# Optimization experiments

Measured on AMD Instinct MI355X. Metric: run time of the kernel, lower is better.

## Reference

```python
import jax, jax.numpy as jnp
import numpy as np

D, H, W = 256, 256, 256
R = 6                      # max_radius: per-Gaussian half-window in voxels


def setup_inputs() -> dict:
    key = jax.random.key(0)
    k1, k2, k3, k4, k5 = jax.random.split(key, 5)
    N = 20000
    center_vox = jax.random.uniform(k1, (N, 3), minval=float(R), maxval=float(D - R), dtype=jnp.float32)
    A = jax.random.normal(k2, (N, 3, 3), dtype=jnp.float32) * 0.5
    # SPD inverse covariance in normalized coords (diffs divided by half_shape ~128)
    cov_inv = (jnp.einsum('nij,nkj->nik', A, A) + jnp.eye(3, dtype=jnp.float32)) * 2000.0
    density_r = jax.random.normal(k3, (N,), dtype=jnp.float32)
    density_i = jax.random.normal(k4, (N,), dtype=jnp.float32)
    radius_vox = jax.random.uniform(k5, (N,), minval=3.0, maxval=float(R), dtype=jnp.float32)
    half_shape = jnp.array([D / 2.0, H / 2.0, W / 2.0], dtype=jnp.float32)
    return {
        'center_vox': center_vox,
        'cov_inv': cov_inv,
        'density_r': density_r,
        'density_i': density_i,
        'radius_vox': radius_vox,
        'half_shape': half_shape,
    }


def reference(center_vox, cov_inv, density_r, density_i, radius_vox, half_shape):
    # Per-Gaussian fixed window of side (2R+1); gather -> Mahalanobis weight -> scatter-add.
    offs = jnp.arange(-R, R + 1, dtype=jnp.int32)
    od, oh, ow = jnp.meshgrid(offs, offs, offs, indexing='ij')
    off = jnp.stack([od, oh, ow], axis=-1).reshape(-1, 3)          # [K3,3]
    base = jnp.floor(center_vox).astype(jnp.int32)                  # [N,3]
    vox = base[:, None, :] + off[None, :, :]                        # [N,K3,3] int
    voxf = vox.astype(center_vox.dtype)
    diff = (voxf - center_vox[:, None, :]) / half_shape             # normalized diff [N,K3,3]
    Md = jnp.einsum('nkd,nde,nke->nk', diff, cov_inv, diff)         # Mahalanobis [N,K3]
    # bbox mask (floor(c-r) .. ceil(c+r)) as in build_tile_pairs / CUDA kernel
    bmin = jnp.floor(center_vox - radius_vox[:, None])
    bmax = jnp.ceil(center_vox + radius_vox[:, None])
    in_bbox = jnp.all((voxf >= bmin[:, None, :]) & (voxf <= bmax[:, None, :]), axis=-1)
    dims = jnp.array([D, H, W], dtype=jnp.int32)
    in_grid = jnp.all((vox >= 0) & (vox < dims), axis=-1)
    mask = (Md <= 9.0) & in_bbox & in_grid
    w = jnp.exp(-0.5 * Md) * mask.astype(Md.dtype)                  # [N,K3]
    flat = jnp.where(in_grid, vox[..., 0] * (H * W) + vox[..., 1] * W + vox[..., 2], 0).reshape(-1)
    vol_r = jnp.zeros(D * H * W, dtype=w.dtype).at[flat].add((w * density_r[:, None]).reshape(-1))
    vol_i = jnp.zeros(D * H * W, dtype=w.dtype).at[flat].add((w * density_i[:, None]).reshape(-1))
    return vol_r.reshape(D, H, W), vol_i.reshape(D, H, W)
```

## Files before the change

kernel.cpp:

```cpp
#include <hip/hip_runtime.h>

#define DD 256
#define HH 256
#define WW 256
#define RMAX 6

#define NTILES 65536
#define CAP 24
#define RECSZ 16
#define OVF_CAP 8192

__global__ __launch_bounds__(256) void fill_kernel(
    const float* __restrict__ center, const float* __restrict__ cov_inv,
    const float* __restrict__ dens_r, const float* __restrict__ dens_i,
    const float* __restrict__ radius, const float* __restrict__ half_shape,
    int* __restrict__ tile_cnt, float* __restrict__ tile_recs,
    int* __restrict__ ovf_cnt, int* __restrict__ ovf_list, int N)
{
    int lane = threadIdx.x & 63;
    int i = __builtin_amdgcn_readfirstlane(blockIdx.x * 4 + (threadIdx.x >> 6));
    if (i >= N) return;

    float cx = center[3*i+0], cy = center[3*i+1], cz = center[3*i+2];
    float r  = radius[i];
    float c00=cov_inv[9*i+0], c01=cov_inv[9*i+1], c02=cov_inv[9*i+2];
    float c11=cov_inv[9*i+4], c12=cov_inv[9*i+5], c22=cov_inv[9*i+8];

    float d00 = c11*c22 - c12*c12;
    float d11 = c00*c22 - c02*c02;
    float d22 = c00*c11 - c01*c01;
    float det = c00*d00 - c01*(c01*c22 - c02*c12) + c02*(c01*c12 - c02*c11);
    float k9  = 9.0f / det;
    float hx = half_shape[0], hy = half_shape[1], hz = half_shape[2];
    float ex = hx * sqrtf(d00 * k9) * 1.0001f + 0.01f;
    float ey = hy * sqrtf(d11 * k9) * 1.0001f + 0.01f;
    float ez = hz * sqrtf(d22 * k9) * 1.0001f + 0.01f;
    float rx = fminf(r, ex), ry = fminf(r, ey), rz = fminf(r, ez);

    int bx=(int)floorf(cx), by=(int)floorf(cy), bz=(int)floorf(cz);
    int xlo = max(max((int)floorf(cx - rx), bx - RMAX), 0);
    int xhi = min(min((int)ceilf (cx + rx), bx + RMAX), DD - 1);
    int ylo = max(max((int)floorf(cy - ry), by - RMAX), 0);
    int yhi = min(min((int)ceilf (cy + ry), by + RMAX), HH - 1);
    int zlo = max(max((int)floorf(cz - rz), bz - RMAX), 0);
    int zhi = min(min((int)ceilf (cz + rz), bz + RMAX), WW - 1);
    if (xlo > xhi || ylo > yhi || zlo > zhi) return;

    int tx0 = xlo >> 2, ntx = (xhi >> 2) - tx0 + 1;
    int ty0 = ylo >> 2, nty = (yhi >> 2) - ty0 + 1;
    int tz0 = zlo >> 4, ntz = (zhi >> 4) - tz0 + 1;
    int ntiles = ntx * nty * ntz;

    if (lane >= ntiles) return;

    unsigned lo = (unsigned)xlo | ((unsigned)ylo << 8) | ((unsigned)zlo << 16);
    unsigned hi = (unsigned)xhi | ((unsigned)yhi << 8) | ((unsigned)zhi << 16);
    float4 r0 = make_float4(cx, cy, cz, c00);
    float4 r1 = make_float4(c11, c22, c01 + c01, c02 + c02);
    float4 r2 = make_float4(c12 + c12, dens_r[i], dens_i[i], __uint_as_float(lo));
    float4 r3 = make_float4(__uint_as_float(hi), 0.f, 0.f, 0.f);

    int t = lane;
    int tzz = tz0 + (t % ntz); t /= ntz;
    int tyy = ty0 + (t % nty); t /= nty;
    int txx = tx0 + t;
    int tile = (txx << 10) | (tyy << 4) | tzz;

    int pos = atomicAdd(&tile_cnt[tile], 1);
    if (pos < CAP) {
        float4* R = (float4*)(tile_recs + ((size_t)tile * CAP + pos) * RECSZ);
        R[0] = r0; R[1] = r1; R[2] = r2; R[3] = r3;
    } else {
        int o = atomicAdd(ovf_cnt, 1);
        if (o < OVF_CAP) { ovf_list[2*o] = tile; ovf_list[2*o+1] = i; }
    }
}

__global__ __launch_bounds__(256) void gather_kernel(
    const int* __restrict__ tile_cnt, const float* __restrict__ tile_recs,
    const float* __restrict__ half_shape,
    float* __restrict__ vol_r, float* __restrict__ vol_i)
{
    __shared__ float4 lds[4 * CAP * 4];
    int w = threadIdx.x >> 6, lane = threadIdx.x & 63;
    int tile = (blockIdx.x << 2) | w;
    int tz = tile & 15, ty = (tile >> 4) & 63, tx = tile >> 10;
    int dxl = lane >> 4, dyl = (lane >> 2) & 3, dzq = lane & 3;
    int vx = tx*4 + dxl, vy = ty*4 + dyl, vz0 = tz*16 + dzq*4;
    float vxf = (float)vx, vyf = (float)vy, vz0f = (float)vz0;
    float ihx = 1.0f/half_shape[0], ihy = 1.0f/half_shape[1], ihz = 1.0f/half_shape[2];

    int n = min(tile_cnt[tile], CAP);
    float4* wl = lds + w * (CAP * 4);
    const float4* src = (const float4*)(tile_recs + (size_t)tile * CAP * RECSZ);
    for (int idx = lane; idx < n * 4; idx += 64) wl[idx] = src[idx];

    float ar0=0.f, ar1=0.f, ar2=0.f, ar3=0.f;
    float ai0=0.f, ai1=0.f, ai2=0.f, ai3=0.f;

    for (int j = 0; j < n; ++j) {
        float4 r0 = wl[j*4+0];
        float4 r1 = wl[j*4+1];
        float4 r2 = wl[j*4+2];
        float4 r3 = wl[j*4+3];
        float cx=r0.x, cy=r0.y, cz=r0.z, s00=r0.w;
        float s11=r1.x, s22=r1.y, s01=r1.z, s02=r1.w;
        float s12=r2.x, dr=r2.y, di=r2.z;
        unsigned lo = __float_as_uint(r2.w), hi = __float_as_uint(r3.x);
        int xlo = lo & 255, ylo = (lo >> 8) & 255, zlo = (lo >> 16) & 255;
        int xhi = hi & 255, yhi = (hi >> 8) & 255, zhi = (hi >> 16) & 255;

        bool okxy = ((unsigned)(vx - xlo) <= (unsigned)(xhi - xlo)) &
                    ((unsigned)(vy - ylo) <= (unsigned)(yhi - ylo));
        int iz0 = vz0 - zlo;
        unsigned zspan = (unsigned)(zhi - zlo);

        float fx = (vxf - cx) * ihx;
        float fy = (vyf - cy) * ihy;
        float axy = fx*fx*s00 + fx*fy*s01 + fy*fy*s11;
        float bxy = fx*s02 + fy*s12;
        float nczihz = -cz * ihz;

        float fz0 = fmaf(vz0f, ihz, nczihz);
        float fz1 = fz0 + ihz;
        float fz2 = fz1 + ihz;
        float fz3 = fz2 + ihz;
        float md0 = fmaf(fz0, fmaf(s22, fz0, bxy), axy);
        float md1 = fmaf(fz1, fmaf(s22, fz1, bxy), axy);
        float md2 = fmaf(fz2, fmaf(s22, fz2, bxy), axy);
        float md3 = fmaf(fz3, fmaf(s22, fz3, bxy), axy);

        bool ok0 = okxy & ((unsigned)(iz0    ) <= zspan) & (md0 <= 9.0f);
        bool ok1 = okxy & ((unsigned)(iz0 + 1) <= zspan) & (md1 <= 9.0f);
        bool ok2 = okxy & ((unsigned)(iz0 + 2) <= zspan) & (md2 <= 9.0f);
        bool ok3 = okxy & ((unsigned)(iz0 + 3) <= zspan) & (md3 <= 9.0f);

        if (__any(ok0 | ok1 | ok2 | ok3)) {
            const float kexp = -0.72134752044448169f;
            float w0 = ok0 ? exp2f(md0 * kexp) : 0.0f;
            float w1 = ok1 ? exp2f(md1 * kexp) : 0.0f;
            float w2 = ok2 ? exp2f(md2 * kexp) : 0.0f;
            float w3 = ok3 ? exp2f(md3 * kexp) : 0.0f;
            ar0 = fmaf(w0, dr, ar0); ai0 = fmaf(w0, di, ai0);
            ar1 = fmaf(w1, dr, ar1); ai1 = fmaf(w1, di, ai1);
            ar2 = fmaf(w2, dr, ar2); ai2 = fmaf(w2, di, ai2);
            ar3 = fmaf(w3, dr, ar3); ai3 = fmaf(w3, di, ai3);
        }
    }

    size_t flat = ((size_t)vx * HH + vy) * WW + vz0;
    *(float4*)(vol_r + flat) = make_float4(ar0, ar1, ar2, ar3);
    *(float4*)(vol_i + flat) = make_float4(ai0, ai1, ai2, ai3);
}

__global__ __launch_bounds__(64) void ovf_kernel(
    const int* __restrict__ ovf_cnt, const int* __restrict__ ovf_list,
    const float* __restrict__ center, const float* __restrict__ cov_inv,
    const float* __restrict__ dens_r, const float* __restrict__ dens_i,
    const float* __restrict__ radius, const float* __restrict__ half_shape,
    float* __restrict__ vol_r, float* __restrict__ vol_i)
{
    int total = min(ovf_cnt[0], OVF_CAP);
    float ihx = 1.0f/half_shape[0], ihy = 1.0f/half_shape[1], ihz = 1.0f/half_shape[2];
    int lane = threadIdx.x;
    for (int p = blockIdx.x; p < total; p += gridDim.x) {
        int tile = ovf_list[2*p], g = ovf_list[2*p+1];
        int tz = tile & 15, ty = (tile >> 4) & 63, tx = tile >> 10;
        int dxl = lane >> 4, dyl = (lane >> 2) & 3, dzq = lane & 3;
        int vx = tx*4 + dxl, vy = ty*4 + dyl, vz0 = tz*16 + dzq*4;

        float cx = center[3*g+0], cy = center[3*g+1], cz = center[3*g+2];
        float r  = radius[g];
        float c00=cov_inv[9*g+0], c01=cov_inv[9*g+1], c02=cov_inv[9*g+2];
        float c10=cov_inv[9*g+3], c11=cov_inv[9*g+4], c12=cov_inv[9*g+5];
        float c20=cov_inv[9*g+6], c21=cov_inv[9*g+7], c22=cov_inv[9*g+8];
        float dr = dens_r[g], di = dens_i[g];

        int bx=(int)floorf(cx), by=(int)floorf(cy), bz=(int)floorf(cz);
        int xlo = max(max((int)floorf(cx - r), bx - RMAX), 0);
        int xhi = min(min((int)ceilf (cx + r), bx + RMAX), DD - 1);
        int ylo = max(max((int)floorf(cy - r), by - RMAX), 0);
        int yhi = min(min((int)ceilf (cy + r), by + RMAX), HH - 1);
        int zlo = max(max((int)floorf(cz - r), bz - RMAX), 0);
        int zhi = min(min((int)ceilf (cz + r), bz + RMAX), WW - 1);

        if (vx < xlo || vx > xhi || vy < ylo || vy > yhi) continue;
        float fx = ((float)vx - cx) * ihx;
        float fy = ((float)vy - cy) * ihy;
        for (int k = 0; k < 4; ++k) {
            int vz = vz0 + k;
            float fz = ((float)vz - cz) * ihz;
            float md = fx*(c00*fx + c01*fy + c02*fz)
                     + fy*(c10*fx + c11*fy + c12*fz)
                     + fz*(c20*fx + c21*fy + c22*fz);
            if (vz >= zlo && vz <= zhi && md <= 9.0f) {
                float wgt = __expf(-0.5f * md);
                size_t flat = ((size_t)vx * HH + vy) * WW + vz;
                atomicAdd(&vol_r[flat], wgt * dr);
                atomicAdd(&vol_i[flat], wgt * di);
            }
        }
    }
}

__global__ __launch_bounds__(256) void splat_kernel(
    const float* __restrict__ center, const float* __restrict__ cov_inv,
    const float* __restrict__ dens_r, const float* __restrict__ dens_i,
    const float* __restrict__ radius, const float* __restrict__ half_shape,
    float* __restrict__ vol_r, float* __restrict__ vol_i, int N)
{
    int g = blockIdx.x;
    if (g >= N) return;
    float cx = center[3*g+0], cy = center[3*g+1], cz = center[3*g+2];
    float r  = radius[g];
    float c00 = cov_inv[9*g+0], c01 = cov_inv[9*g+1], c02 = cov_inv[9*g+2];
    float c10 = cov_inv[9*g+3], c11 = cov_inv[9*g+4], c12 = cov_inv[9*g+5];
    float c20 = cov_inv[9*g+6], c21 = cov_inv[9*g+7], c22 = cov_inv[9*g+8];
    float dr = dens_r[g], di = dens_i[g];
    float ihx = 1.0f/half_shape[0], ihy = 1.0f/half_shape[1], ihz = 1.0f/half_shape[2];
    int bx = (int)floorf(cx), by = (int)floorf(cy), bz = (int)floorf(cz);
    int xlo = max(max((int)floorf(cx - r), bx - RMAX), 0);
    int xhi = min(min((int)ceilf (cx + r), bx + RMAX), DD - 1);
    int ylo = max(max((int)floorf(cy - r), by - RMAX), 0);
    int yhi = min(min((int)ceilf (cy + r), by + RMAX), HH - 1);
    int zlo = max(max((int)floorf(cz - r), bz - RMAX), 0);
    int zhi = min(min((int)ceilf (cz + r), bz + RMAX), WW - 1);
    int nx = xhi-xlo+1, ny = yhi-ylo+1, nz = zhi-zlo+1;
    if (nx <= 0 || ny <= 0 || nz <= 0) return;
    int total = nx*ny*nz;
    for (int k = threadIdx.x; k < total; k += 256) {
        int iz = k % nz, tq = k / nz, iy = tq % ny, ix = tq / ny;
        int vx = xlo+ix, vy = ylo+iy, vz = zlo+iz;
        float dxn = ((float)vx - cx) * ihx;
        float dyn = ((float)vy - cy) * ihy;
        float dzn = ((float)vz - cz) * ihz;
        float md = dxn*(c00*dxn + c01*dyn + c02*dzn)
                 + dyn*(c10*dxn + c11*dyn + c12*dzn)
                 + dzn*(c20*dxn + c21*dyn + c22*dzn);
        if (md <= 9.0f) {
            float wgt = __expf(-0.5f*md);
            int flat = (vx*HH + vy)*WW + vz;
            atomicAdd(&vol_r[flat], wgt*dr);
            atomicAdd(&vol_i[flat], wgt*di);
        }
    }
}

extern "C" void kernel_launch(void* const* d_in, const int* in_sizes, int n_in,
                              void* d_out, int out_size, void* d_ws, size_t ws_size,
                              hipStream_t stream) {
    const float* center     = (const float*)d_in[0];
    const float* cov_inv    = (const float*)d_in[1];
    const float* dens_r     = (const float*)d_in[2];
    const float* dens_i     = (const float*)d_in[3];
    const float* radius     = (const float*)d_in[4];
    const float* half_shape = (const float*)d_in[5];
    int N = in_sizes[0] / 3;

    float* vol_r = (float*)d_out;
    float* vol_i = vol_r + (size_t)DD * HH * WW;

    size_t rec_floats = (size_t)NTILES * CAP * RECSZ;
    size_t need = rec_floats * sizeof(float)
                + ((size_t)NTILES + 4 + 2*OVF_CAP) * sizeof(int);
    if (ws_size < need) {
        (void)hipMemsetAsync(d_out, 0, (size_t)out_size * sizeof(float), stream);
        splat_kernel<<<N, 256, 0, stream>>>(center, cov_inv, dens_r, dens_i,
                                            radius, half_shape, vol_r, vol_i, N);
        return;
    }

    float* tile_recs = (float*)d_ws;
    int*   tile_cnt  = (int*)(tile_recs + rec_floats);
    int*   ovf_cnt   = tile_cnt + NTILES;
    int*   ovf_list  = ovf_cnt + 4;

    (void)hipMemsetAsync(tile_cnt, 0, ((size_t)NTILES + 4) * sizeof(int), stream);
    fill_kernel<<<(N + 3)/4, 256, 0, stream>>>(center, cov_inv, dens_r, dens_i,
                                               radius, half_shape,
                                               tile_cnt, tile_recs,
                                               ovf_cnt, ovf_list, N);
    gather_kernel<<<NTILES/4, 256, 0, stream>>>(tile_cnt, tile_recs, half_shape,
                                                vol_r, vol_i);
    ovf_kernel<<<64, 64, 0, stream>>>(ovf_cnt, ovf_list, center, cov_inv,
                                      dens_r, dens_i, radius, half_shape,
                                      vol_r, vol_i);
}
```

Before: 205.9 us.

## Fuse overflow handling into gather kernel and pack two Gaussians per wave in fill

Removes the separate overflow kernel launch and folds its work into the gather kernel, where each tile scans the overflow list and accumulates matching entries in registers instead of issuing atomics. The fill kernel now assigns 32 lanes per Gaussian, so each wave handles two Gaussians and launches half as many blocks. The gather kernel also issues the first record load before reading the tile count. The trade-off is that every tile linearly scans the whole overflow list when it is non-empty, and a Gaussian spanning more than 32 tiles would lose its extra tiles.

```diff
diff --git a/kernel.cpp b/kernel.cpp
--- a/kernel.cpp
+++ b/kernel.cpp
@@ -17,8 +17,8 @@
     int* __restrict__ tile_cnt, float* __restrict__ tile_recs,
     int* __restrict__ ovf_cnt, int* __restrict__ ovf_list, int N)
 {
-    int lane = threadIdx.x & 63;
-    int i = __builtin_amdgcn_readfirstlane(blockIdx.x * 4 + (threadIdx.x >> 6));
+    int lane32 = threadIdx.x & 31;
+    int i = blockIdx.x * 8 + (threadIdx.x >> 5);
     if (i >= N) return;
 
     float cx = center[3*i+0], cy = center[3*i+1], cz = center[3*i+2];
@@ -51,7 +51,7 @@
     int tz0 = zlo >> 4, ntz = (zhi >> 4) - tz0 + 1;
     int ntiles = ntx * nty * ntz;
 
-    if (lane >= ntiles) return;
+    if (lane32 >= ntiles) return;
 
     unsigned lo = (unsigned)xlo | ((unsigned)ylo << 8) | ((unsigned)zlo << 16);
     unsigned hi = (unsigned)xhi | ((unsigned)yhi << 8) | ((unsigned)zhi << 16);
@@ -60,7 +60,7 @@
     float4 r2 = make_float4(c12 + c12, dens_r[i], dens_i[i], __uint_as_float(lo));
     float4 r3 = make_float4(__uint_as_float(hi), 0.f, 0.f, 0.f);
 
-    int t = lane;
+    int t = lane32;
     int tzz = tz0 + (t % ntz); t /= ntz;
     int tyy = ty0 + (t % nty); t /= nty;
     int txx = tx0 + t;
@@ -79,6 +79,10 @@
 __global__ __launch_bounds__(256) void gather_kernel(
     const int* __restrict__ tile_cnt, const float* __restrict__ tile_recs,
     const float* __restrict__ half_shape,
+    const int* __restrict__ ovf_cnt, const int* __restrict__ ovf_list,
+    const float* __restrict__ center, const float* __restrict__ cov_inv,
+    const float* __restrict__ dens_r, const float* __restrict__ dens_i,
+    const float* __restrict__ radius,
     float* __restrict__ vol_r, float* __restrict__ vol_i)
 {
     __shared__ float4 lds[4 * CAP * 4];
@@ -90,10 +94,13 @@
     float vxf = (float)vx, vyf = (float)vy, vz0f = (float)vz0;
     float ihx = 1.0f/half_shape[0], ihy = 1.0f/half_shape[1], ihz = 1.0f/half_shape[2];
 
-    int n = min(tile_cnt[tile], CAP);
     float4* wl = lds + w * (CAP * 4);
     const float4* src = (const float4*)(tile_recs + (size_t)tile * CAP * RECSZ);
-    for (int idx = lane; idx < n * 4; idx += 64) wl[idx] = src[idx];
+
+    if (lane < 16) wl[lane] = src[lane];
+    int ocnt = min(ovf_cnt[0], OVF_CAP);
+    int n = min(tile_cnt[tile], CAP);
+    for (int idx = 16 + lane; idx < n * 4; idx += 64) wl[idx] = src[idx];
 
     float ar0=0.f, ar1=0.f, ar2=0.f, ar3=0.f;
     float ai0=0.f, ai1=0.f, ai2=0.f, ai3=0.f;
@@ -148,59 +155,46 @@
         }
     }
 
+    if (ocnt > 0) {
+        for (int p = 0; p < ocnt; ++p) {
+            if (ovf_list[2*p] != tile) continue;
+            int g = ovf_list[2*p+1];
+            float cx = center[3*g+0], cy = center[3*g+1], cz = center[3*g+2];
+            float r  = radius[g];
+            float c00=cov_inv[9*g+0], c01=cov_inv[9*g+1], c02=cov_inv[9*g+2];
+            float c11=cov_inv[9*g+4], c12=cov_inv[9*g+5], c22=cov_inv[9*g+8];
+            float dr = dens_r[g], di = dens_i[g];
+            int bx=(int)floorf(cx), by=(int)floorf(cy), bz=(int)floorf(cz);
+            int xlo = max(max((int)floorf(cx - r), bx - RMAX), 0);
+            int xhi = min(min((int)ceilf (cx + r), bx + RMAX), DD - 1);
+            int ylo = max(max((int)floorf(cy - r), by - RMAX), 0);
+            int yhi = min(min((int)ceilf (cy + r), by + RMAX), HH - 1);
+            int zlo = max(max((int)floorf(cz - r), bz - RMAX), 0);
+            int zhi = min(min((int)ceilf (cz + r), bz + RMAX), WW - 1);
+            if (vx < xlo || vx > xhi || vy < ylo || vy > yhi) continue;
+            float fx = (vxf - cx) * ihx;
+            float fy = (vyf - cy) * ihy;
+            float axy = fx*fx*c00 + 2.0f*fx*fy*c01 + fy*fy*c11;
+            float bxy = 2.0f*(fx*c02 + fy*c12);
+            #pragma unroll
+            for (int k = 0; k < 4; ++k) {
+                int vz = vz0 + k;
+                float fz = ((float)vz - cz) * ihz;
+                float md = fmaf(fz, fmaf(c22, fz, bxy), axy);
+                if (vz >= zlo && vz <= zhi && md <= 9.0f) {
+                    float wgt = __expf(-0.5f * md);
+                    if (k == 0) { ar0 = fmaf(wgt, dr, ar0); ai0 = fmaf(wgt, di, ai0); }
+                    if (k == 1) { ar1 = fmaf(wgt, dr, ar1); ai1 = fmaf(wgt, di, ai1); }
+                    if (k == 2) { ar2 = fmaf(wgt, dr, ar2); ai2 = fmaf(wgt, di, ai2); }
+                    if (k == 3) { ar3 = fmaf(wgt, dr, ar3); ai3 = fmaf(wgt, di, ai3); }
+                }
+            }
+        }
+    }
+
     size_t flat = ((size_t)vx * HH + vy) * WW + vz0;
     *(float4*)(vol_r + flat) = make_float4(ar0, ar1, ar2, ar3);
     *(float4*)(vol_i + flat) = make_float4(ai0, ai1, ai2, ai3);
-}
-
-__global__ __launch_bounds__(64) void ovf_kernel(
-    const int* __restrict__ ovf_cnt, const int* __restrict__ ovf_list,
-    const float* __restrict__ center, const float* __restrict__ cov_inv,
-    const float* __restrict__ dens_r, const float* __restrict__ dens_i,
-    const float* __restrict__ radius, const float* __restrict__ half_shape,
-    float* __restrict__ vol_r, float* __restrict__ vol_i)
-{
-    int total = min(ovf_cnt[0], OVF_CAP);
-    float ihx = 1.0f/half_shape[0], ihy = 1.0f/half_shape[1], ihz = 1.0f/half_shape[2];
-    int lane = threadIdx.x;
-    for (int p = blockIdx.x; p < total; p += gridDim.x) {
-        int tile = ovf_list[2*p], g = ovf_list[2*p+1];
-        int tz = tile & 15, ty = (tile >> 4) & 63, tx = tile >> 10;
-        int dxl = lane >> 4, dyl = (lane >> 2) & 3, dzq = lane & 3;
-        int vx = tx*4 + dxl, vy = ty*4 + dyl, vz0 = tz*16 + dzq*4;
-
-        float cx = center[3*g+0], cy = center[3*g+1], cz = center[3*g+2];
-        float r  = radius[g];
-        float c00=cov_inv[9*g+0], c01=cov_inv[9*g+1], c02=cov_inv[9*g+2];
-        float c10=cov_inv[9*g+3], c11=cov_inv[9*g+4], c12=cov_inv[9*g+5];
-        float c20=cov_inv[9*g+6], c21=cov_inv[9*g+7], c22=cov_inv[9*g+8];
-        float dr = dens_r[g], di = dens_i[g];
-
-        int bx=(int)floorf(cx), by=(int)floorf(cy), bz=(int)floorf(cz);
-        int xlo = max(max((int)floorf(cx - r), bx - RMAX), 0);
-        int xhi = min(min((int)ceilf (cx + r), bx + RMAX), DD - 1);
-        int ylo = max(max((int)floorf(cy - r), by - RMAX), 0);
-        int yhi = min(min((int)ceilf (cy + r), by + RMAX), HH - 1);
-        int zlo = max(max((int)floorf(cz - r), bz - RMAX), 0);
-        int zhi = min(min((int)ceilf (cz + r), bz + RMAX), WW - 1);
-
-        if (vx < xlo || vx > xhi || vy < ylo || vy > yhi) continue;
-        float fx = ((float)vx - cx) * ihx;
-        float fy = ((float)vy - cy) * ihy;
-        for (int k = 0; k < 4; ++k) {
-            int vz = vz0 + k;
-            float fz = ((float)vz - cz) * ihz;
-            float md = fx*(c00*fx + c01*fy + c02*fz)
-                     + fy*(c10*fx + c11*fy + c12*fz)
-                     + fz*(c20*fx + c21*fy + c22*fz);
-            if (vz >= zlo && vz <= zhi && md <= 9.0f) {
-                float wgt = __expf(-0.5f * md);
-                size_t flat = ((size_t)vx * HH + vy) * WW + vz;
-                atomicAdd(&vol_r[flat], wgt * dr);
-                atomicAdd(&vol_i[flat], wgt * di);
-            }
-        }
-    }
 }
 
 __global__ __launch_bounds__(256) void splat_kernel(
@@ -276,13 +270,12 @@
     int*   ovf_list  = ovf_cnt + 4;
 
     (void)hipMemsetAsync(tile_cnt, 0, ((size_t)NTILES + 4) * sizeof(int), stream);
-    fill_kernel<<<(N + 3)/4, 256, 0, stream>>>(center, cov_inv, dens_r, dens_i,
+    fill_kernel<<<(N + 7)/8, 256, 0, stream>>>(center, cov_inv, dens_r, dens_i,
                                                radius, half_shape,
                                                tile_cnt, tile_recs,
                                                ovf_cnt, ovf_list, N);
     gather_kernel<<<NTILES/4, 256, 0, stream>>>(tile_cnt, tile_recs, half_shape,
-                                                vol_r, vol_i);
-    ovf_kernel<<<64, 64, 0, stream>>>(ovf_cnt, ovf_list, center, cov_inv,
-                                      dens_r, dens_i, radius, half_shape,
-                                      vol_r, vol_i);
-}
+                                                ovf_cnt, ovf_list,
+                                                center, cov_inv, dens_r, dens_i,
+                                                radius, vol_r, vol_i);
+}
```

Result: slower. 210.7 us (+2.3%).
